# Kernel tuning notes

Measured on AMD Instinct MI355X. Metric: run time of the kernel, lower is better.

Reference implementation:

```python
import jax, jax.numpy as jnp
import numpy as np

N_NODES = 100000
N_EDGES = 3200000
IN_CH, H1, H2, N_CLS = 128, 32, 20, 10
EPS = 1e-12  # F.normalize eps


def _glorot(key, shape):
    fan_in = shape[0]
    return jax.random.normal(key, shape, dtype=jnp.float32) / np.sqrt(fan_in)


def setup_inputs() -> dict:
    key = jax.random.key(0)
    ks = jax.random.split(key, 9)
    x = jax.random.normal(ks[0], (N_NODES, IN_CH), dtype=jnp.float32)
    edge_index = jax.random.randint(ks[1], (2, N_EDGES), 0, N_NODES, dtype=jnp.int64)
    return {
        "x": x,
        "edge_index": edge_index,
        "W1_l": _glorot(ks[2], (IN_CH, H1)),
        "b1_l": jnp.zeros((H1,), jnp.float32),
        "W1_r": _glorot(ks[3], (IN_CH, H1)),
        "W2_l": _glorot(ks[4], (H1, H2)),
        "b2_l": jnp.zeros((H2,), jnp.float32),
        "W2_r": _glorot(ks[5], (H1, H2)),
        "W_out": _glorot(ks[6], (H2, N_CLS)),
        "b_out": jnp.zeros((N_CLS,), jnp.float32),
    }


def _sage_conv(x, src, dst, W_l, b_l, W_r, n_nodes):
    # mean-aggregate neighbor features: scatter x[src] into dst buckets
    agg = jax.ops.segment_sum(x[src], dst, num_segments=n_nodes)  # [N, F]
    deg = jax.ops.segment_sum(jnp.ones((src.shape[0], 1), x.dtype), dst,
                              num_segments=n_nodes)
    agg = agg / jnp.maximum(deg, 1.0)
    out = agg @ W_l + b_l + x @ W_r  # lin_l(agg) + lin_r(x), lin_r has no bias
    # normalize=True -> L2 normalize per node
    nrm = jnp.maximum(jnp.linalg.norm(out, axis=-1, keepdims=True), EPS)
    return out / nrm


def reference(x, edge_index, W1_l, b1_l, W1_r, W2_l, b2_l, W2_r, W_out, b_out):
    src, dst = edge_index[0], edge_index[1]
    n = x.shape[0]
    h = _sage_conv(x, src, dst, W1_l, b1_l, W1_r, n)
    h = jax.nn.relu(h)
    # dropout(p=0.5) is identity in eval mode
    h = _sage_conv(h, src, dst, W2_l, b2_l, W2_r, n)
    logits = h @ W_out + b_out
    return jax.nn.softmax(logits, axis=1)
```

## Files before the change

kernel.cpp:

```cpp
#include <hip/hip_runtime.h>
#include <hip/hip_fp16.h>
#include <math.h>


#define BSHIFT 7
#define BS_NODES 128
#define PART_TILE 4096

__global__ __launch_bounds__(256) void k_lin1(
    const float* __restrict__ x, const float* __restrict__ W1l,
    const float* __restrict__ W1r, __half* __restrict__ y1,
    float* __restrict__ r1, int n_nodes)
{
    int n = blockIdx.x * 256 + threadIdx.x;
    if (n >= n_nodes) return;
    float accL[32], accR[32];
#pragma unroll
    for (int j = 0; j < 32; ++j) { accL[j] = 0.f; accR[j] = 0.f; }
    const float4* x4 = reinterpret_cast<const float4*>(x) + (size_t)n * 32;
    for (int k4 = 0; k4 < 32; ++k4) {
        float4 xv = x4[k4];
        const float* wl = W1l + k4 * 4 * 32;
        const float* wr = W1r + k4 * 4 * 32;
#pragma unroll
        for (int j = 0; j < 32; ++j) {
            float a = accL[j];
            a = fmaf(xv.x, wl[j],      a);
            a = fmaf(xv.y, wl[32 + j], a);
            a = fmaf(xv.z, wl[64 + j], a);
            a = fmaf(xv.w, wl[96 + j], a);
            accL[j] = a;
            float b = accR[j];
            b = fmaf(xv.x, wr[j],      b);
            b = fmaf(xv.y, wr[32 + j], b);
            b = fmaf(xv.z, wr[64 + j], b);
            b = fmaf(xv.w, wr[96 + j], b);
            accR[j] = b;
        }
    }
    unsigned upk[16];
#pragma unroll
    for (int q = 0; q < 16; ++q) {
        __half2 h = __floats2half2_rn(accL[2*q], accL[2*q+1]);
        upk[q] = *reinterpret_cast<unsigned*>(&h);
    }
    uint4* yo = reinterpret_cast<uint4*>(y1 + (size_t)n * 32);
#pragma unroll
    for (int q = 0; q < 4; ++q)
        yo[q] = make_uint4(upk[4*q], upk[4*q+1], upk[4*q+2], upk[4*q+3]);
    float4* ro = reinterpret_cast<float4*>(r1 + (size_t)n * 32);
#pragma unroll
    for (int q = 0; q < 8; ++q)
        ro[q] = make_float4(accR[q*4], accR[q*4+1], accR[q*4+2], accR[q*4+3]);
}

__global__ __launch_bounds__(256) void k_binit(
    int* __restrict__ bcursor, int nb, int capb)
{
    int i = blockIdx.x * 256 + threadIdx.x;
    if (i < nb) bcursor[i] = i * capb;
}

__global__ __launch_bounds__(256) void k_part(
    const int* __restrict__ src, const int* __restrict__ dst,
    int* __restrict__ bcursor, int* __restrict__ pairs,
    int n_edges, int nb)
{
    __shared__ int cnt[1024];
    __shared__ int bbase_l[1024];
    int tid = threadIdx.x;
    int ebeg = blockIdx.x * PART_TILE;
    int eend = ebeg + PART_TILE; if (eend > n_edges) eend = n_edges;
    for (int i = tid; i < nb; i += 256) cnt[i] = 0;
    __syncthreads();
    for (int e = ebeg + tid; e < eend; e += 256)
        atomicAdd(&cnt[dst[e] >> BSHIFT], 1);
    __syncthreads();
    for (int i = tid; i < nb; i += 256) {
        int c = cnt[i];
        if (c > 0) bbase_l[i] = atomicAdd(&bcursor[i], c);
    }
    __syncthreads();
    for (int e = ebeg + tid; e < eend; e += 256) {
        int d = dst[e];
        int b = d >> BSHIFT;
        int slot = atomicSub(&cnt[b], 1) - 1;
        pairs[(size_t)bbase_l[b] + slot] = (src[e] << BSHIFT) | (d & (BS_NODES - 1));
    }
}

__global__ __launch_bounds__(1024) void k_bscan(
    const int* __restrict__ bcursor, int* __restrict__ bbase,
    int* __restrict__ row_ptr, int nb, int capb, int n_nodes)
{
    __shared__ int sc[1024];
    int t = threadIdx.x;
    int c = (t < nb) ? (bcursor[t] - t * capb) : 0;
    sc[t] = c;
    __syncthreads();
    for (int off = 1; off < 1024; off <<= 1) {
        int v = (t >= off) ? sc[t - off] : 0;
        __syncthreads();
        sc[t] += v;
        __syncthreads();
    }
    if (t < nb) bbase[t] = sc[t] - c;
    if (t == 1023) row_ptr[n_nodes] = sc[t];
}

__global__ __launch_bounds__(256) void k_bfill(
    const int* __restrict__ pairs, const int* __restrict__ bcursor,
    const int* __restrict__ bbase, int* __restrict__ row_ptr,
    int* __restrict__ eid, int capb, int n_nodes)
{
    __shared__ int cnt128[BS_NODES];
    __shared__ int sc[BS_NODES];
    __shared__ int cur[BS_NODES];
    int b = blockIdx.x;
    int t = threadIdx.x;
    int lo = b * BS_NODES;
    size_t pbeg = (size_t)b * capb;
    int cntE = bcursor[b] - b * capb;
    int base = bbase[b];
    if (t < BS_NODES) cnt128[t] = 0;
    __syncthreads();
    for (int i = t; i < cntE; i += 256)
        atomicAdd(&cnt128[pairs[pbeg + i] & (BS_NODES - 1)], 1);
    __syncthreads();
    int myc = 0;
    if (t < BS_NODES) { myc = cnt128[t]; sc[t] = myc; }
    __syncthreads();
    for (int off = 1; off < BS_NODES; off <<= 1) {
        int v = (t >= off && t < BS_NODES) ? sc[t - off] : 0;
        __syncthreads();
        if (t < BS_NODES) sc[t] += v;
        __syncthreads();
    }
    if (t < BS_NODES) {
        int excl = sc[t] - myc;
        cur[t] = excl;
        if (lo + t < n_nodes) row_ptr[lo + t] = base + excl;
    }
    __syncthreads();
    for (int i = t; i < cntE; i += 256) {
        int p = pairs[pbeg + i];
        int pos = atomicAdd(&cur[p & (BS_NODES - 1)], 1);
        eid[(size_t)base + pos] = p >> BSHIFT;
    }
}

__device__ __forceinline__ float gather_sum(
    const int* __restrict__ eid, const __half* __restrict__ tab,
    int beg, int end, int ch)
{
    float s0 = 0.f, s1 = 0.f, s2 = 0.f, s3 = 0.f;
    float s4 = 0.f, s5 = 0.f, s6 = 0.f, s7 = 0.f;
    int i = beg;
    for (; i + 8 <= end; i += 8) {
        int e0 = eid[i];
        int e1 = eid[i + 1];
        int e2 = eid[i + 2];
        int e3 = eid[i + 3];
        int e4 = eid[i + 4];
        int e5 = eid[i + 5];
        int e6 = eid[i + 6];
        int e7 = eid[i + 7];
        s0 += __half2float(tab[(size_t)e0 * 32 + ch]);
        s1 += __half2float(tab[(size_t)e1 * 32 + ch]);
        s2 += __half2float(tab[(size_t)e2 * 32 + ch]);
        s3 += __half2float(tab[(size_t)e3 * 32 + ch]);
        s4 += __half2float(tab[(size_t)e4 * 32 + ch]);
        s5 += __half2float(tab[(size_t)e5 * 32 + ch]);
        s6 += __half2float(tab[(size_t)e6 * 32 + ch]);
        s7 += __half2float(tab[(size_t)e7 * 32 + ch]);
    }
    for (; i + 4 <= end; i += 4) {
        int e0 = eid[i];
        int e1 = eid[i + 1];
        int e2 = eid[i + 2];
        int e3 = eid[i + 3];
        s0 += __half2float(tab[(size_t)e0 * 32 + ch]);
        s1 += __half2float(tab[(size_t)e1 * 32 + ch]);
        s2 += __half2float(tab[(size_t)e2 * 32 + ch]);
        s3 += __half2float(tab[(size_t)e3 * 32 + ch]);
    }
    for (; i < end; ++i) {
        int e = eid[i];
        s0 += __half2float(tab[(size_t)e * 32 + ch]);
    }
    return ((s0 + s1) + (s2 + s3)) + ((s4 + s5) + (s6 + s7));
}

__global__ __launch_bounds__(256) void k_agg1(
    const int* __restrict__ row_ptr, const int* __restrict__ eid,
    const __half* __restrict__ y1, const float* __restrict__ r1,
    const float* __restrict__ b1, const float* __restrict__ W2l,
    const float* __restrict__ W2r,
    __half* __restrict__ z2, float* __restrict__ r2, int n_nodes)
{
    int t = blockIdx.x * 256 + threadIdx.x;
    int n = t >> 5;
    int ch = t & 31;
    if (n >= n_nodes) return;
    int beg = row_ptr[n], end = row_ptr[n + 1];
    float sum = gather_sum(eid, y1, beg, end, ch);
    float inv = 1.0f / fmaxf((float)(end - beg), 1.0f);
    float v = fmaf(sum, inv, b1[ch] + r1[(size_t)n * 32 + ch]);
    float ss = v * v;
#pragma unroll
    for (int off = 16; off >= 1; off >>= 1) ss += __shfl_xor(ss, off, 32);
    float h = fmaxf(v / fmaxf(sqrtf(ss), 1e-12f), 0.f);
    float accl = 0.f, accr = 0.f;
#pragma unroll 4
    for (int ii = 0; ii < 32; ++ii) {
        float hv = __shfl(h, ii, 32);
        if (ch < 20) {
            accl = fmaf(hv, W2l[ii * 20 + ch], accl);
            accr = fmaf(hv, W2r[ii * 20 + ch], accr);
        }
    }
    z2[(size_t)n * 32 + ch] = __float2half(ch < 20 ? accl : 0.f);
    if (ch < 20) r2[(size_t)n * 20 + ch] = accr;
}

__global__ __launch_bounds__(256) void k_agg2(
    const int* __restrict__ row_ptr, const int* __restrict__ eid,
    const __half* __restrict__ z2, const float* __restrict__ r2,
    const float* __restrict__ b2, const float* __restrict__ Wout,
    const float* __restrict__ bout,
    float* __restrict__ out, int n_nodes)
{
    int t = blockIdx.x * 256 + threadIdx.x;
    int n = t >> 5;
    int ch = t & 31;
    if (n >= n_nodes) return;
    int beg = row_ptr[n], end = row_ptr[n + 1];
    bool act = ch < 20;
    float sum = gather_sum(eid, z2, beg, end, ch);
    float inv = 1.0f / fmaxf((float)(end - beg), 1.0f);
    float v = act ? fmaf(sum, inv, b2[ch] + r2[(size_t)n * 20 + ch]) : 0.f;
    float ss = v * v;
#pragma unroll
    for (int off = 16; off >= 1; off >>= 1) ss += __shfl_xor(ss, off, 32);
    float o = v / fmaxf(sqrtf(ss), 1e-12f);
    float acc = (ch < 10) ? bout[ch] : 0.f;
#pragma unroll 4
    for (int ii = 0; ii < 20; ++ii) {
        float ov = __shfl(o, ii, 32);
        if (ch < 10) acc = fmaf(ov, Wout[ii * 10 + ch], acc);
    }
    float lm = (ch < 10) ? acc : -1e30f;
    float m = lm;
#pragma unroll
    for (int off = 8; off >= 1; off >>= 1) m = fmaxf(m, __shfl_xor(m, off, 16));
    float ex = (ch < 10) ? expf(acc - m) : 0.f;
    float s2r = ex;
#pragma unroll
    for (int off = 8; off >= 1; off >>= 1) s2r += __shfl_xor(s2r, off, 16);
    if (ch < 10) out[(size_t)n * 10 + ch] = ex / s2r;
}

extern "C" void kernel_launch(void* const* d_in, const int* in_sizes, int n_in,
                              void* d_out, int out_size, void* d_ws, size_t ws_size,
                              hipStream_t stream)
{
    const float* x    = (const float*)d_in[0];
    const int*   ei   = (const int*)d_in[1];
    const float* W1l  = (const float*)d_in[2];
    const float* b1   = (const float*)d_in[3];
    const float* W1r  = (const float*)d_in[4];
    const float* W2l  = (const float*)d_in[5];
    const float* b2   = (const float*)d_in[6];
    const float* W2r  = (const float*)d_in[7];
    const float* Wout = (const float*)d_in[8];
    const float* bout = (const float*)d_in[9];
    float* out = (float*)d_out;

    int n_nodes = in_sizes[0] / 128;
    int n_edges = in_sizes[1] / 2;
    const int* src = ei;
    const int* dst = ei + n_edges;

    int nb = (n_nodes + BS_NODES - 1) / BS_NODES;
    double mean = (double)n_edges / nb;
    int capb = (int)(mean + 8.0 * sqrt(mean) + 64.0);
    capb = (capb + 63) & ~63;

    int* bcursor = (int*)d_ws;
    int* bbase   = bcursor + ((nb + 2 + 3) & ~3);
    int* row_ptr = bbase + ((nb + 3) & ~3);
    int* eid     = row_ptr + (((n_nodes + 1) + 3) & ~3);
    int* pairs   = eid + (((size_t)n_edges + 3) & ~(size_t)3);

    __half* y1 = (__half*)pairs;
    float*  r1 = (float*)(y1 + (size_t)n_nodes * 32);
    __half* z2 = (__half*)(r1 + (size_t)n_nodes * 32);
    float*  r2 = (float*)(z2 + (size_t)n_nodes * 32);

    int nb_part = (n_edges + PART_TILE - 1) / PART_TILE;
    int nb_node = (n_nodes + 255) / 256;
    int nb_grp  = ((n_nodes * 32) + 255) / 256;

    k_binit<<<(nb + 255) / 256, 256, 0, stream>>>(bcursor, nb, capb);
    k_part<<<nb_part, 256, 0, stream>>>(src, dst, bcursor, pairs, n_edges, nb);
    k_bscan<<<1, 1024, 0, stream>>>(bcursor, bbase, row_ptr, nb, capb, n_nodes);
    k_bfill<<<nb, 256, 0, stream>>>(pairs, bcursor, bbase, row_ptr, eid, capb, n_nodes);
    k_lin1<<<nb_node, 256, 0, stream>>>(x, W1l, W1r, y1, r1, n_nodes);
    k_agg1<<<nb_grp, 256, 0, stream>>>(row_ptr, eid, y1, r1, b1, W2l, W2r, z2, r2, n_nodes);
    k_agg2<<<nb_grp, 256, 0, stream>>>(row_ptr, eid, z2, r2, b2, Wout, bout, out, n_nodes);
}
```

Before: 330.4 us.

## Stage x through LDS in k_lin1, store root terms in fp16, fold biases

k_lin1 now loads x rows cooperatively and coalesced into LDS as packed fp16 with a rotated (swizzled) layout, then each thread computes its node from LDS. Before, each thread made strided float4 reads of its own row. The root-term buffers r1/r2 become fp16 with the biases folded in, which cuts intermediate traffic, and r2 is padded to 32 channels. PART_TILE is doubled for the partition kernel. Converting x to fp16 before the matmul lowers input precision, and the 64KB LDS per block limits occupancy.

```diff
diff --git a/kernel.cpp b/kernel.cpp
--- a/kernel.cpp
+++ b/kernel.cpp
@@ -5,53 +5,11 @@
 
 #define BSHIFT 7
 #define BS_NODES 128
-#define PART_TILE 4096
-
-__global__ __launch_bounds__(256) void k_lin1(
-    const float* __restrict__ x, const float* __restrict__ W1l,
-    const float* __restrict__ W1r, __half* __restrict__ y1,
-    float* __restrict__ r1, int n_nodes)
-{
-    int n = blockIdx.x * 256 + threadIdx.x;
-    if (n >= n_nodes) return;
-    float accL[32], accR[32];
-#pragma unroll
-    for (int j = 0; j < 32; ++j) { accL[j] = 0.f; accR[j] = 0.f; }
-    const float4* x4 = reinterpret_cast<const float4*>(x) + (size_t)n * 32;
-    for (int k4 = 0; k4 < 32; ++k4) {
-        float4 xv = x4[k4];
-        const float* wl = W1l + k4 * 4 * 32;
-        const float* wr = W1r + k4 * 4 * 32;
-#pragma unroll
-        for (int j = 0; j < 32; ++j) {
-            float a = accL[j];
-            a = fmaf(xv.x, wl[j],      a);
-            a = fmaf(xv.y, wl[32 + j], a);
-            a = fmaf(xv.z, wl[64 + j], a);
-            a = fmaf(xv.w, wl[96 + j], a);
-            accL[j] = a;
-            float b = accR[j];
-            b = fmaf(xv.x, wr[j],      b);
-            b = fmaf(xv.y, wr[32 + j], b);
-            b = fmaf(xv.z, wr[64 + j], b);
-            b = fmaf(xv.w, wr[96 + j], b);
-            accR[j] = b;
-        }
-    }
-    unsigned upk[16];
-#pragma unroll
-    for (int q = 0; q < 16; ++q) {
-        __half2 h = __floats2half2_rn(accL[2*q], accL[2*q+1]);
-        upk[q] = *reinterpret_cast<unsigned*>(&h);
-    }
-    uint4* yo = reinterpret_cast<uint4*>(y1 + (size_t)n * 32);
-#pragma unroll
-    for (int q = 0; q < 4; ++q)
-        yo[q] = make_uint4(upk[4*q], upk[4*q+1], upk[4*q+2], upk[4*q+3]);
-    float4* ro = reinterpret_cast<float4*>(r1 + (size_t)n * 32);
-#pragma unroll
-    for (int q = 0; q < 8; ++q)
-        ro[q] = make_float4(accR[q*4], accR[q*4+1], accR[q*4+2], accR[q*4+3]);
+#define PART_TILE 8192
+
+__device__ __forceinline__ unsigned pk(float a, float b) {
+    __half2 h = __floats2half2_rn(a, b);
+    return *reinterpret_cast<unsigned*>(&h);
 }
 
 __global__ __launch_bounds__(256) void k_binit(
@@ -146,6 +104,68 @@
         int p = pairs[pbeg + i];
         int pos = atomicAdd(&cur[p & (BS_NODES - 1)], 1);
         eid[(size_t)base + pos] = p >> BSHIFT;
+    }
+}
+
+__global__ __launch_bounds__(256) void k_lin1(
+    const float* __restrict__ x, const float* __restrict__ W1l,
+    const float* __restrict__ b1, const float* __restrict__ W1r,
+    __half* __restrict__ y1, __half* __restrict__ r1, int n_nodes)
+{
+    __shared__ unsigned lds[256 * 64];
+    int tid = threadIdx.x;
+    int base = blockIdx.x * 256;
+    const float4* x4 = reinterpret_cast<const float4*>(x);
+#pragma unroll
+    for (int it = 0; it < 32; ++it) {
+        int f = it * 256 + tid;
+        int row = f >> 5, c4 = f & 31;
+        int node = base + row;
+        float4 v = make_float4(0.f, 0.f, 0.f, 0.f);
+        if (node < n_nodes) v = x4[(size_t)node * 32 + c4];
+        int kk = c4 * 2;
+        lds[row * 64 + ((kk + row) & 63)]     = pk(v.x, v.y);
+        lds[row * 64 + ((kk + 1 + row) & 63)] = pk(v.z, v.w);
+    }
+    __syncthreads();
+    int node = base + tid;
+    float accL[32], accR[32];
+#pragma unroll
+    for (int j = 0; j < 32; ++j) { accL[j] = 0.f; accR[j] = 0.f; }
+    const unsigned* rb = &lds[tid * 64];
+    for (int kk = 0; kk < 64; ++kk) {
+        unsigned u = rb[(kk + tid) & 63];
+        __half2 hh = *reinterpret_cast<__half2*>(&u);
+        float2 f = __half22float2(hh);
+        const float* wl = W1l + kk * 64;
+        const float* wr = W1r + kk * 64;
+#pragma unroll
+        for (int j = 0; j < 32; ++j) {
+            float a = accL[j];
+            a = fmaf(f.x, wl[j],      a);
+            a = fmaf(f.y, wl[32 + j], a);
+            accL[j] = a;
+            float c = accR[j];
+            c = fmaf(f.x, wr[j],      c);
+            c = fmaf(f.y, wr[32 + j], c);
+            accR[j] = c;
+        }
+    }
+    if (node < n_nodes) {
+        unsigned o[16];
+#pragma unroll
+        for (int q = 0; q < 16; ++q) o[q] = pk(accL[2*q], accL[2*q+1]);
+        uint4* yo = reinterpret_cast<uint4*>(y1 + (size_t)node * 32);
+#pragma unroll
+        for (int q = 0; q < 4; ++q)
+            yo[q] = make_uint4(o[4*q], o[4*q+1], o[4*q+2], o[4*q+3]);
+#pragma unroll
+        for (int q = 0; q < 16; ++q)
+            o[q] = pk(accR[2*q] + b1[2*q], accR[2*q+1] + b1[2*q+1]);
+        uint4* ro = reinterpret_cast<uint4*>(r1 + (size_t)node * 32);
+#pragma unroll
+        for (int q = 0; q < 4; ++q)
+            ro[q] = make_uint4(o[4*q], o[4*q+1], o[4*q+2], o[4*q+3]);
     }
 }
 
@@ -193,10 +213,10 @@
 
 __global__ __launch_bounds__(256) void k_agg1(
     const int* __restrict__ row_ptr, const int* __restrict__ eid,
-    const __half* __restrict__ y1, const float* __restrict__ r1,
-    const float* __restrict__ b1, const float* __restrict__ W2l,
-    const float* __restrict__ W2r,
-    __half* __restrict__ z2, float* __restrict__ r2, int n_nodes)
+    const __half* __restrict__ y1, const __half* __restrict__ r1,
+    const float* __restrict__ W2l, const float* __restrict__ W2r,
+    const float* __restrict__ b2,
+    __half* __restrict__ z2, __half* __restrict__ r2, int n_nodes)
 {
     int t = blockIdx.x * 256 + threadIdx.x;
     int n = t >> 5;
@@ -205,7 +225,7 @@
     int beg = row_ptr[n], end = row_ptr[n + 1];
     float sum = gather_sum(eid, y1, beg, end, ch);
     float inv = 1.0f / fmaxf((float)(end - beg), 1.0f);
-    float v = fmaf(sum, inv, b1[ch] + r1[(size_t)n * 32 + ch]);
+    float v = fmaf(sum, inv, __half2float(r1[(size_t)n * 32 + ch]));
     float ss = v * v;
 #pragma unroll
     for (int off = 16; off >= 1; off >>= 1) ss += __shfl_xor(ss, off, 32);
@@ -220,14 +240,13 @@
         }
     }
     z2[(size_t)n * 32 + ch] = __float2half(ch < 20 ? accl : 0.f);
-    if (ch < 20) r2[(size_t)n * 20 + ch] = accr;
+    r2[(size_t)n * 32 + ch] = __float2half(ch < 20 ? accr + b2[ch] : 0.f);
 }
 
 __global__ __launch_bounds__(256) void k_agg2(
     const int* __restrict__ row_ptr, const int* __restrict__ eid,
-    const __half* __restrict__ z2, const float* __restrict__ r2,
-    const float* __restrict__ b2, const float* __restrict__ Wout,
-    const float* __restrict__ bout,
+    const __half* __restrict__ z2, const __half* __restrict__ r2,
+    const float* __restrict__ Wout, const float* __restrict__ bout,
     float* __restrict__ out, int n_nodes)
 {
     int t = blockIdx.x * 256 + threadIdx.x;
@@ -238,7 +257,7 @@
     bool act = ch < 20;
     float sum = gather_sum(eid, z2, beg, end, ch);
     float inv = 1.0f / fmaxf((float)(end - beg), 1.0f);
-    float v = act ? fmaf(sum, inv, b2[ch] + r2[(size_t)n * 20 + ch]) : 0.f;
+    float v = act ? fmaf(sum, inv, __half2float(r2[(size_t)n * 32 + ch])) : 0.f;
     float ss = v * v;
 #pragma unroll
     for (int off = 16; off >= 1; off >>= 1) ss += __shfl_xor(ss, off, 32);
@@ -293,9 +312,9 @@
     int* pairs   = eid + (((size_t)n_edges + 3) & ~(size_t)3);
 
     __half* y1 = (__half*)pairs;
-    float*  r1 = (float*)(y1 + (size_t)n_nodes * 32);
-    __half* z2 = (__half*)(r1 + (size_t)n_nodes * 32);
-    float*  r2 = (float*)(z2 + (size_t)n_nodes * 32);
+    __half* r1 = y1 + (size_t)n_nodes * 32;
+    __half* z2 = r1 + (size_t)n_nodes * 32;
+    __half* r2 = z2 + (size_t)n_nodes * 32;
 
     int nb_part = (n_edges + PART_TILE - 1) / PART_TILE;
     int nb_node = (n_nodes + 255) / 256;
@@ -305,7 +324,7 @@
     k_part<<<nb_part, 256, 0, stream>>>(src, dst, bcursor, pairs, n_edges, nb);
     k_bscan<<<1, 1024, 0, stream>>>(bcursor, bbase, row_ptr, nb, capb, n_nodes);
     k_bfill<<<nb, 256, 0, stream>>>(pairs, bcursor, bbase, row_ptr, eid, capb, n_nodes);
-    k_lin1<<<nb_node, 256, 0, stream>>>(x, W1l, W1r, y1, r1, n_nodes);
-    k_agg1<<<nb_grp, 256, 0, stream>>>(row_ptr, eid, y1, r1, b1, W2l, W2r, z2, r2, n_nodes);
-    k_agg2<<<nb_grp, 256, 0, stream>>>(row_ptr, eid, z2, r2, b2, Wout, bout, out, n_nodes);
-}
+    k_lin1<<<nb_node, 256, 0, stream>>>(x, W1l, b1, W1r, y1, r1, n_nodes);
+    k_agg1<<<nb_grp, 256, 0, stream>>>(row_ptr, eid, y1, r1, W2l, W2r, b2, z2, r2, n_nodes);
+    k_agg2<<<nb_grp, 256, 0, stream>>>(row_ptr, eid, z2, r2, Wout, bout, out, n_nodes);
+}
```

Result: faster. 322.8 us (-2.3%).
